# Kernel optimization log

Hardware: AMD Instinct MI355X
Metric: run time of the kernel (lower is better)

Reference implementation:

```python
import jax, jax.numpy as jnp
import numpy as np

# Factor graph dims
D = 5            # state_dimensions: variables per factor
S = 2 ** D       # factor_state_space = 32
F = 100000       # numFactors
V = 60000        # numVars
E = F * D        # edges: one per (factor, incident variable)
ALPHA = 0.5      # residual weight on factorToVar messages
ALPHA2 = 0.5     # residual weight around MLPs
NEG = -1e30      # -inf surrogate, grad-safe


def setup_inputs() -> dict:
    key = jax.random.key(0)
    ks = jax.random.split(key, 5)
    prv_varToFactor_messages = jax.random.normal(ks[0], (E, 2), jnp.float32)
    prv_factorToVar_messages = jax.random.normal(ks[1], (E, 2), jnp.float32)
    prv_factor_beliefs = jax.random.normal(ks[2], (F, S), jnp.float32)  # log-space beliefs, flattened [2]*D
    factor_potentials = jax.random.normal(ks[3], (F, S), jnp.float32)
    # each factor has exactly D incident edges; edge e's variable occupies dim edge_var_dim[e] of the factor tensor
    edge_f = jnp.repeat(jnp.arange(F, dtype=jnp.int32), D)
    edge_v = jax.random.randint(ks[4], (E,), 0, V, dtype=jnp.int32)
    edge_var_dim = jnp.tile(jnp.arange(D, dtype=jnp.int32), F)
    eye = jnp.eye(S, dtype=jnp.float32)  # torch init: identity weights, zero bias
    z = jnp.zeros((S,), jnp.float32)
    return dict(prv_varToFactor_messages=prv_varToFactor_messages,
                prv_factorToVar_messages=prv_factorToVar_messages,
                prv_factor_beliefs=prv_factor_beliefs,
                factor_potentials=factor_potentials,
                W1=eye, b1=z, W2=eye, b2=z, W3=eye, b3=z, W4=eye, b4=z,
                edge_f=edge_f, edge_v=edge_v, edge_var_dim=edge_var_dim)


def reference(prv_varToFactor_messages, prv_factorToVar_messages, prv_factor_beliefs,
              factor_potentials, W1, b1, W2, b2, W3, b3, W4, b4,
              edge_f, edge_v, edge_var_dim):
    # idx_grid[d, s] = bit of flattened state s along factor dim d (binary vars)
    idx_grid = ((jnp.arange(S)[None, :] >> (D - 1 - jnp.arange(D))[:, None]) & 1)  # [D, S]
    sel = idx_grid[edge_var_dim]  # [E, S]: per-edge coordinate of its variable in each factor state

    # ---- factor -> var messages (map_beliefs gather + no-double-counting subtract + multi-axis logsumexp)
    mapped_fb = prv_factor_beliefs[edge_f]                                        # [E, S] gather
    adj = mapped_fb - jnp.take_along_axis(prv_varToFactor_messages, sel, axis=1)  # divide out prv v->f msg
    mask = sel[:, None, :] == jnp.arange(2)[None, :, None]                         # [E, 2, S]
    f2v = jax.nn.logsumexp(jnp.where(mask, adj[:, None, :], NEG), axis=2)          # marginalize other dims -> [E,2]
    f2v = ALPHA * f2v + (1.0 - ALPHA) * prv_factorToVar_messages                   # residual
    f2v = f2v - jax.nn.logsumexp(f2v, axis=1, keepdims=True)                       # normalize messages

    # ---- var beliefs = scatter_add of incoming messages
    var_beliefs = jax.ops.segment_sum(f2v, edge_v, num_segments=V)                 # [V, 2]

    # ---- var -> factor messages (subtract just-sent f->v message)
    v2f = var_beliefs[edge_v] - f2v
    v2f = v2f - jax.nn.logsumexp(v2f, axis=1, keepdims=True)

    # ---- expand v->f messages to full factor state space and run MLP1 (log-space, lne_mlp=False)
    v2f_expand = jnp.take_along_axis(v2f, sel, axis=1)                              # [E, S]
    h1 = (v2f_expand @ W1.T + b1) @ W2.T + b2
    v2f_expand = ALPHA2 * h1 + (1.0 - ALPHA2) * v2f_expand

    # ---- factor beliefs = potentials + scatter_add of expanded messages, then MLP2
    factor_beliefs = factor_potentials + jax.ops.segment_sum(v2f_expand, edge_f, num_segments=F)  # [F, S]
    h2 = (factor_beliefs @ W3.T + b3) @ W4.T + b4
    factor_beliefs = ALPHA2 * h2 + (1.0 - ALPHA2) * factor_beliefs

    return v2f, f2v, factor_beliefs, var_beliefs
```

## Files before the change

### kernel.cpp

```cpp
#include <hip/hip_runtime.h>

#define DD 5
#define SS 32
#define F_N 100000
#define V_N 60000
#define E_N (F_N * DD)
#define NB_EDGE 1954


__device__ __forceinline__ float lse2(float a, float b) {
    float m = fmaxf(a, b);
    return m + __logf(__expf(a - m) + __expf(b - m));
}

__device__ __forceinline__ float2 dec_vb(unsigned long long x) {
    float cnt = (float)(unsigned)(x >> 56);
    float a1  = (float)(int)((x >> 28) & 0xFFFFFFFu) * (1.f/8192.f) - 64.f * cnt;
    float a0  = (float)(int)(x & 0xFFFFFFFu)         * (1.f/8192.f) - 64.f * cnt;
    return make_float2(a0, a1);
}

__global__ __launch_bounds__(256) void k_f2v(
    const float* __restrict__ prv_v2f,
    const float* __restrict__ prv_f2v,
    const float* __restrict__ prv_fb,
    const int*   __restrict__ edge_v,
    const float* __restrict__ W1, const float* __restrict__ b1,
    const float* __restrict__ W2, const float* __restrict__ b2,
    const float* __restrict__ W3, const float* __restrict__ b3,
    const float* __restrict__ W4, const float* __restrict__ b4,
    float* __restrict__ ws,
    unsigned long long* __restrict__ acc,
    float* __restrict__ out_f2v)
{
    const int t = threadIdx.x;

    if (blockIdx.x == NB_EDGE) {
        __shared__ float sE1[SS*SS], sE2[SS*SS], sM[SS*SS], sb1e[SS];
        for (int idx = t; idx < SS*SS; idx += 256) {
            const int i = idx >> 5, k = idx & 31;
            float a1 = 0.f, a2 = 0.f;
            #pragma unroll
            for (int j = 0; j < SS; ++j) {
                a1 += W2[i*SS+j] * W1[j*SS+k];
                a2 += W4[i*SS+j] * W3[j*SS+k];
            }
            sE1[idx] = 0.5f*a1 + (i == k ? 0.5f : 0.f);
            sE2[idx] = 0.5f*a2 + (i == k ? 0.5f : 0.f);
        }
        if (t < SS) {
            float a = 0.f;
            #pragma unroll
            for (int j = 0; j < SS; ++j) a += W2[t*SS+j] * b1[j];
            sb1e[t] = 0.5f * (a + b2[t]);
        }
        __syncthreads();
        for (int idx = t; idx < SS*SS; idx += 256) {
            const int i = idx >> 5, k = idx & 31;
            float m = 0.f;
            #pragma unroll
            for (int j = 0; j < SS; ++j) m += sE2[i*SS+j] * sE1[j*SS+k];
            sM[idx] = m;
            ws[idx] = sE2[idx];
        }
        __syncthreads();
        if (t < SS) {
            float u = 0.f, wb[DD] = {0.f,0.f,0.f,0.f,0.f};
            #pragma unroll
            for (int s = 0; s < SS; ++s) {
                float m = sM[t*SS+s];
                u += m;
                #pragma unroll
                for (int d = 0; d < DD; ++d) if ((s >> (4-d)) & 1) wb[d] += m;
            }
            ws[1024+t] = u;
            #pragma unroll
            for (int d = 0; d < DD; ++d) ws[1056 + t*DD + d] = wb[d];
            float cv = 0.f, bb = 0.f;
            #pragma unroll
            for (int j = 0; j < SS; ++j) {
                cv += sE2[t*SS+j] * sb1e[j];
                bb += W4[t*SS+j] * b3[j];
            }
            ws[1216+t] = 5.f*cv + 0.5f*(bb + b4[t]);
        }
        return;
    }

    const int e = blockIdx.x * 256 + t;
    if (e >= E_N) return;
    const int f = e / DD;
    const int d = e - f * DD;
    const int shift = 4 - d;

    float fb[SS];
    const float4* rp = (const float4*)(prv_fb + (size_t)f * SS);
    #pragma unroll
    for (int i = 0; i < 8; ++i) {
        float4 v = rp[i];
        fb[4*i+0] = v.x; fb[4*i+1] = v.y; fb[4*i+2] = v.z; fb[4*i+3] = v.w;
    }
    float M = fb[0];
    #pragma unroll
    for (int s = 1; s < SS; ++s) M = fmaxf(M, fb[s]);
    float s0 = 0.f, s1 = 0.f;
    #pragma unroll
    for (int s = 0; s < SS; ++s) {
        float E = __expf(fb[s] - M);
        if ((s >> shift) & 1) s1 += E; else s0 += E;
    }
    float L0 = M + __logf(s0);
    float L1 = M + __logf(s1);

    float2 m = ((const float2*)prv_v2f)[e];
    float2 p = ((const float2*)prv_f2v)[e];
    float a0 = 0.5f * (L0 - m.x) + 0.5f * p.x;
    float a1 = 0.5f * (L1 - m.y) + 0.5f * p.y;
    float z = lse2(a0, a1);
    a0 -= z; a1 -= z;
    ((float2*)out_f2v)[e] = make_float2(a0, a1);

    const int q0 = __float2int_rn((a0 + 64.f) * 8192.f);
    const int q1 = __float2int_rn((a1 + 64.f) * 8192.f);
    unsigned long long enc = (1ULL << 56) | ((unsigned long long)q1 << 28)
                           | (unsigned long long)q0;
    atomicAdd(acc + edge_v[e], enc);
}

__global__ __launch_bounds__(256) void k_fb(
    const float* __restrict__ pot,
    const int*   __restrict__ edge_v,
    const float* __restrict__ f2v,
    const unsigned long long* __restrict__ acc,
    const float* __restrict__ ws,
    float* __restrict__ out_v2f,
    float* __restrict__ out_fb,
    float* __restrict__ out_vb)
{
    __shared__ float sW[SS*33], su[SS], sB[SS*DD], sc[SS];
    const int t = threadIdx.x;
    for (int idx = t; idx < SS*SS; idx += 256)
        sW[(idx>>5)*33 + (idx&31)] = ws[idx];
    if (t < 32)                 su[t]     = ws[1024 + t];
    else if (t < 64)            sc[t-32]  = ws[1216 + (t-32)];
    else if (t < 64 + SS*DD)    sB[t-64]  = ws[1056 + (t-64)];

    const int vid = blockIdx.x * 256 + t;
    if (vid < V_N)
        ((float2*)out_vb)[vid] = dec_vb(acc[vid]);

    __syncthreads();

    const int f = blockIdx.x * 8 + (t >> 5);
    const int i = t & 31;

    float c = 0.f, dl[DD], w0[DD], w1[DD];
    #pragma unroll
    for (int d = 0; d < DD; ++d) {
        int e = f * DD + d;
        float2 m = ((const float2*)f2v)[e];
        float2 B = dec_vb(acc[edge_v[e]]);
        float a0 = B.x - m.x, a1 = B.y - m.y;
        float z = lse2(a0, a1);
        a0 -= z; a1 -= z;
        c += a0; dl[d] = a1 - a0;
        w0[d] = a0; w1[d] = a1;
    }
    if (i < DD)
        ((float2*)out_v2f)[f*DD + i] = make_float2(w0[i], w1[i]);

    float acc_o = sc[i] + c * su[i];
    #pragma unroll
    for (int d = 0; d < DD; ++d) acc_o += sB[i*DD+d] * dl[d];
    const float4* pp = (const float4*)(pot + (size_t)f * SS);
    #pragma unroll
    for (int q = 0; q < 8; ++q) {
        float4 pv = pp[q];
        acc_o += sW[i*33+4*q+0]*pv.x + sW[i*33+4*q+1]*pv.y
               + sW[i*33+4*q+2]*pv.z + sW[i*33+4*q+3]*pv.w;
    }
    out_fb[(size_t)f*SS + i] = acc_o;
}

extern "C" void kernel_launch(void* const* d_in, const int* in_sizes, int n_in,
                              void* d_out, int out_size, void* d_ws, size_t ws_size,
                              hipStream_t stream) {
    const float* prv_v2f = (const float*)d_in[0];
    const float* prv_f2v = (const float*)d_in[1];
    const float* prv_fb  = (const float*)d_in[2];
    const float* pot     = (const float*)d_in[3];
    const float* W1 = (const float*)d_in[4];
    const float* b1 = (const float*)d_in[5];
    const float* W2 = (const float*)d_in[6];
    const float* b2 = (const float*)d_in[7];
    const float* W3 = (const float*)d_in[8];
    const float* b3 = (const float*)d_in[9];
    const float* W4 = (const float*)d_in[10];
    const float* b4 = (const float*)d_in[11];
    const int* edge_v = (const int*)d_in[13];

    float* out   = (float*)d_out;
    float* o_v2f = out;
    float* o_f2v = out + 2*(size_t)E_N;
    float* o_fb  = out + 4*(size_t)E_N;
    float* o_vb  = o_fb + (size_t)F_N * SS;
    float* ws    = (float*)d_ws;
    unsigned long long* acc = (unsigned long long*)((char*)d_ws + 8192);

    hipMemsetAsync(acc, 0, (size_t)V_N * sizeof(unsigned long long), stream);

    k_f2v<<<NB_EDGE + 1, 256, 0, stream>>>(prv_v2f, prv_f2v, prv_fb, edge_v,
                                           W1, b1, W2, b2, W3, b3, W4, b4,
                                           ws, acc, o_f2v);

    k_fb<<<F_N / 8, 256, 0, stream>>>(pot, edge_v, o_f2v, acc, ws,
                                      o_v2f, o_fb, o_vb);
}
```

Measured before the change: 168.8 us.

## Deduplicate per-edge v2f work in factor-belief kernel and keep weights in registers

The factor-belief kernel now handles 64 factors per block instead of 8. Each edge's var-to-factor normalization (gather of the accumulated var belief, decode, logsumexp) is computed once by one thread and staged in shared memory, rather than recomputed by all 32 lanes of the factor's warp. Per-factor payloads (sum and bit deltas) are reduced once. Each thread then keeps its row of the fused 32x32 weight matrix and bias terms in registers and reuses them across 8 factors. The workspace layout is padded so those rows can be read as float4. In exchange the kernel has two extra block barriers, fewer blocks, and more registers per thread.

```diff
diff --git a/kernel.cpp b/kernel.cpp
--- a/kernel.cpp
+++ b/kernel.cpp
@@ -6,6 +6,8 @@
 #define V_N 60000
 #define E_N (F_N * DD)
 #define NB_EDGE 1954
+#define FB_FPB 64
+#define FB_T 256
 
 
 __device__ __forceinline__ float lse2(float a, float b) {
@@ -18,6 +20,10 @@
     float a1  = (float)(int)((x >> 28) & 0xFFFFFFFu) * (1.f/8192.f) - 64.f * cnt;
     float a0  = (float)(int)(x & 0xFFFFFFFu)         * (1.f/8192.f) - 64.f * cnt;
     return make_float2(a0, a1);
+}
+
+__device__ __forceinline__ float dot4(float4 a, float4 b) {
+    return a.x*b.x + a.y*b.y + a.z*b.z + a.w*b.w;
 }
 
 __global__ __launch_bounds__(256) void k_f2v(
@@ -75,14 +81,14 @@
             }
             ws[1024+t] = u;
             #pragma unroll
-            for (int d = 0; d < DD; ++d) ws[1056 + t*DD + d] = wb[d];
+            for (int d = 0; d < DD; ++d) ws[1088 + t*8 + d] = wb[d];
             float cv = 0.f, bb = 0.f;
             #pragma unroll
             for (int j = 0; j < SS; ++j) {
                 cv += sE2[t*SS+j] * sb1e[j];
                 bb += W4[t*SS+j] * b3[j];
             }
-            ws[1216+t] = 5.f*cv + 0.5f*(bb + b4[t]);
+            ws[1056+t] = 5.f*cv + 0.5f*(bb + b4[t]);
         }
         return;
     }
@@ -127,7 +133,7 @@
     atomicAdd(acc + edge_v[e], enc);
 }
 
-__global__ __launch_bounds__(256) void k_fb(
+__global__ __launch_bounds__(FB_T) void k_fb(
     const float* __restrict__ pot,
     const int*   __restrict__ edge_v,
     const float* __restrict__ f2v,
@@ -137,49 +143,65 @@
     float* __restrict__ out_fb,
     float* __restrict__ out_vb)
 {
-    __shared__ float sW[SS*33], su[SS], sB[SS*DD], sc[SS];
+    __shared__ float2 sa[FB_FPB*DD];
+    __shared__ float  sPay[FB_FPB*8];
     const int t = threadIdx.x;
-    for (int idx = t; idx < SS*SS; idx += 256)
-        sW[(idx>>5)*33 + (idx&31)] = ws[idx];
-    if (t < 32)                 su[t]     = ws[1024 + t];
-    else if (t < 64)            sc[t-32]  = ws[1216 + (t-32)];
-    else if (t < 64 + SS*DD)    sB[t-64]  = ws[1056 + (t-64)];
-
-    const int vid = blockIdx.x * 256 + t;
+    const int fbase = blockIdx.x * FB_FPB;
+    const int nf = min(FB_FPB, F_N - fbase);
+    const int ne = nf * DD;
+
+    const int vid = blockIdx.x * FB_T + t;
     if (vid < V_N)
         ((float2*)out_vb)[vid] = dec_vb(acc[vid]);
 
-    __syncthreads();
-
-    const int f = blockIdx.x * 8 + (t >> 5);
-    const int i = t & 31;
-
-    float c = 0.f, dl[DD], w0[DD], w1[DD];
-    #pragma unroll
-    for (int d = 0; d < DD; ++d) {
-        int e = f * DD + d;
+    for (int le = t; le < ne; le += FB_T) {
+        const int e = fbase * DD + le;
         float2 m = ((const float2*)f2v)[e];
         float2 B = dec_vb(acc[edge_v[e]]);
         float a0 = B.x - m.x, a1 = B.y - m.y;
         float z = lse2(a0, a1);
         a0 -= z; a1 -= z;
-        c += a0; dl[d] = a1 - a0;
-        w0[d] = a0; w1[d] = a1;
-    }
-    if (i < DD)
-        ((float2*)out_v2f)[f*DD + i] = make_float2(w0[i], w1[i]);
-
-    float acc_o = sc[i] + c * su[i];
-    #pragma unroll
-    for (int d = 0; d < DD; ++d) acc_o += sB[i*DD+d] * dl[d];
-    const float4* pp = (const float4*)(pot + (size_t)f * SS);
-    #pragma unroll
-    for (int q = 0; q < 8; ++q) {
-        float4 pv = pp[q];
-        acc_o += sW[i*33+4*q+0]*pv.x + sW[i*33+4*q+1]*pv.y
-               + sW[i*33+4*q+2]*pv.z + sW[i*33+4*q+3]*pv.w;
-    }
-    out_fb[(size_t)f*SS + i] = acc_o;
+        ((float2*)out_v2f)[e] = make_float2(a0, a1);
+        sa[le] = make_float2(a0, a1);
+    }
+    __syncthreads();
+    if (t < nf) {
+        float2 e0 = sa[t*DD+0], e1 = sa[t*DD+1], e2 = sa[t*DD+2],
+               e3 = sa[t*DD+3], e4 = sa[t*DD+4];
+        sPay[t*8+0] = e0.x + e1.x + e2.x + e3.x + e4.x;
+        sPay[t*8+1] = e0.y - e0.x;
+        sPay[t*8+2] = e1.y - e1.x;
+        sPay[t*8+3] = e2.y - e2.x;
+        sPay[t*8+4] = e3.y - e3.x;
+        sPay[t*8+5] = e4.y - e4.x;
+        sPay[t*8+6] = 0.f; sPay[t*8+7] = 0.f;
+    }
+    __syncthreads();
+
+    const int g = t >> 5, i = t & 31;
+    const float4* wr = (const float4*)(ws + (size_t)i * SS);
+    const float4 w0 = wr[0], w1 = wr[1], w2 = wr[2], w3 = wr[3],
+                 w4 = wr[4], w5 = wr[5], w6 = wr[6], w7 = wr[7];
+    const float4* br = (const float4*)(ws + 1088 + (size_t)i * 8);
+    const float4 bA = br[0], bB = br[1];
+    const float ui  = ws[1024 + i];
+    const float c32 = ws[1056 + i];
+
+    #pragma unroll
+    for (int j = 0; j < 8; ++j) {
+        const int fl = g * 8 + j;
+        if (fl >= nf) break;
+        const int f = fbase + fl;
+        const float4 pay0 = ((const float4*)sPay)[fl*2];
+        const float4 pay1 = ((const float4*)sPay)[fl*2 + 1];
+        float acc_o = c32 + pay0.x * ui
+                    + bA.x*pay0.y + bA.y*pay0.z + bA.z*pay0.w
+                    + bA.w*pay1.x + bB.x*pay1.y;
+        const float4* pp = (const float4*)(pot + (size_t)f * SS);
+        acc_o += dot4(w0, pp[0]) + dot4(w1, pp[1]) + dot4(w2, pp[2]) + dot4(w3, pp[3])
+               + dot4(w4, pp[4]) + dot4(w5, pp[5]) + dot4(w6, pp[6]) + dot4(w7, pp[7]);
+        out_fb[(size_t)f * SS + i] = acc_o;
+    }
 }
 
 extern "C" void kernel_launch(void* const* d_in, const int* in_sizes, int n_in,
@@ -213,6 +235,7 @@
                                            W1, b1, W2, b2, W3, b3, W4, b4,
                                            ws, acc, o_f2v);
 
-    k_fb<<<F_N / 8, 256, 0, stream>>>(pot, edge_v, o_f2v, acc, ws,
-                                      o_v2f, o_fb, o_vb);
-}
+    const int blocks2 = (F_N + FB_FPB - 1) / FB_FPB;
+    k_fb<<<blocks2, FB_T, 0, stream>>>(pot, edge_v, o_f2v, acc, ws,
+                                       o_v2f, o_fb, o_vb);
+}
```

After: 158.1 us. 1.07x faster.
